# Kernel optimization log

Hardware: AMD Instinct MI355X
Metric: run time of the kernel (lower is better)

Reference implementation:

```python
import jax, jax.numpy as jnp
import numpy as np

N_EMBD = 1024
N_HEAD = 16
R = 16
SCALING = 1.0 / 16.0  # loralib default lora_alpha=1, scaling = alpha/r


def lora_linear(x, W, b, A, B):
    # loralib: y = x @ W.T + b + (x @ A.T) @ B.T * scaling
    return x @ W.T + b + (x @ A.T) @ B.T * SCALING


def setup_inputs() -> dict:
    key = jax.random.key(0)
    ks = jax.random.split(key, 16)
    B, T, S, C = 8, 1024, 256, N_EMBD
    std = 0.02
    return {
        "x": jax.random.normal(ks[0], (B, T, C), jnp.float32),
        "feature": jax.random.normal(ks[1], (B, S, C), jnp.float32),
        # c_attn (q projection)
        "Wq": jax.random.normal(ks[2], (C, C), jnp.float32) * std,
        "bq": jnp.zeros((C,), jnp.float32),
        "Aq": jax.random.normal(ks[3], (R, C), jnp.float32) * std,
        "Bq": jnp.zeros((C, R), jnp.float32),
        # feature_attn (kv projection)
        "Wf": jax.random.normal(ks[4], (2 * C, C), jnp.float32) * std,
        "bf": jnp.zeros((2 * C,), jnp.float32),
        "Af": jax.random.normal(ks[5], (R, C), jnp.float32) * std,
        "Bf": jnp.zeros((2 * C, R), jnp.float32),
        # c_proj
        "Wp": jax.random.normal(ks[6], (C, C), jnp.float32) * std,
        "bp": jnp.zeros((C,), jnp.float32),
        "Ap": jax.random.normal(ks[7], (R, C), jnp.float32) * std,
        "Bp": jnp.zeros((C, R), jnp.float32),
    }


def reference(x, feature, Wq, bq, Aq, Bq, Wf, bf, Af, Bf, Wp, bp, Ap, Bp):
    Bsz, T, C = x.shape
    S = feature.shape[1]
    H = N_HEAD
    D = C // H

    q = lora_linear(x, Wq, bq, Aq, Bq).reshape(Bsz, T, H, D).transpose(0, 2, 1, 3)
    kv = lora_linear(feature, Wf, bf, Af, Bf)
    k, v = kv[..., :C], kv[..., C:]
    k = k.reshape(Bsz, S, H, D).transpose(0, 2, 1, 3)
    v = v.reshape(Bsz, S, H, D).transpose(0, 2, 1, 3)

    att = jnp.einsum("bhtd,bhsd->bhts", q, k) * (1.0 / np.sqrt(D))
    mask = jnp.tril(jnp.ones((T, S), bool))  # bias[:, :, :T, :S]
    att = jnp.where(mask, att, -jnp.inf)
    att = jax.nn.softmax(att, axis=-1)

    y = jnp.einsum("bhts,bhsd->bhtd", att, v)
    y = y.transpose(0, 2, 1, 3).reshape(Bsz, T, C)
    return lora_linear(y, Wp, bp, Ap, Bp)
```

## Files before the change

### kernel.cpp

```cpp
#include <hip/hip_runtime.h>
#include <hip/hip_bf16.h>
#include <stdint.h>
#include <stddef.h>

typedef __hip_bfloat16 bf16;
typedef __attribute__((ext_vector_type(8))) short short8;
typedef __attribute__((ext_vector_type(4))) float floatx4;

__device__ __forceinline__ void async_load16(const bf16* g, bf16* l) {
#if defined(__has_builtin) && __has_builtin(__builtin_amdgcn_global_load_lds)
  __builtin_amdgcn_global_load_lds((__attribute__((address_space(1))) void*)g,
                                   (__attribute__((address_space(3))) void*)l,
                                   16, 0, 0);
#else
  *(short8*)l = *(const short8*)g;
#endif
}

__device__ __forceinline__ int wave_detect_f32(const unsigned short* __restrict__ xr) {
  const int lane = threadIdx.x & 63;
  const unsigned short u = xr[lane];
  const int e = (u >> 7) & 0xFF;
  const unsigned long long m = __ballot(e >= 0x93);
  return (__popcll(m) > 5) ? 1 : 0;
}

__device__ __forceinline__ float ldf(const void* p, int i, int flg) {
  return flg ? ((const float*)p)[i] : __bfloat162float(((const bf16*)p)[i]);
}

struct PrepArgs {
  const void *x, *ft, *bq, *bf, *bp;
  const void *Wq, *Aq, *Bq, *Wf, *Af, *Bf, *Wp, *Ap, *Bp;
  bf16 *cx, *cft, *cbq, *cbf, *cbp, *weffq, *wefff, *weffp;
};

__device__ __forceinline__ void canon4(const void* src, bf16* dst, int i4, int flg) {
  if (flg) {
    const float4 v = ((const float4*)src)[i4];
    dst[i4 * 4 + 0] = __float2bfloat16(v.x);
    dst[i4 * 4 + 1] = __float2bfloat16(v.y);
    dst[i4 * 4 + 2] = __float2bfloat16(v.z);
    dst[i4 * 4 + 3] = __float2bfloat16(v.w);
  } else {
    ((uint2*)dst)[i4] = ((const uint2*)src)[i4];
  }
}

__device__ __forceinline__ void weff1(const void* W, const void* Bm, const void* Am,
                                      bf16* dst, int idx, int flg) {
  const int n = idx >> 10, k = idx & 1023;
  float acc = 0.f;
#pragma unroll
  for (int r = 0; r < 16; ++r)
    acc += ldf(Bm, n * 16 + r, flg) * ldf(Am, r * 1024 + k, flg);
  dst[idx] = __float2bfloat16(ldf(W, idx, flg) + 0.0625f * acc);
}

__global__ __launch_bounds__(256) void prep_kernel(PrepArgs a) {
  const int flg = wave_detect_f32((const unsigned short*)a.x);
  const int bid = blockIdx.x, tid = threadIdx.x;
  if (bid < 8192) {
    canon4(a.x, a.cx, bid * 256 + tid, flg);
  } else if (bid < 10240) {
    canon4(a.ft, a.cft, (bid - 8192) * 256 + tid, flg);
  } else if (bid < 10241) {
    canon4(a.bq, a.cbq, tid, flg);
  } else if (bid < 10243) {
    canon4(a.bf, a.cbf, (bid - 10241) * 256 + tid, flg);
  } else if (bid < 10244) {
    canon4(a.bp, a.cbp, tid, flg);
  } else if (bid < 14340) {
    weff1(a.Wq, a.Bq, a.Aq, a.weffq, (bid - 10244) * 256 + tid, flg);
  } else if (bid < 22532) {
    weff1(a.Wf, a.Bf, a.Af, a.wefff, (bid - 14340) * 256 + tid, flg);
  } else {
    weff1(a.Wp, a.Bp, a.Ap, a.weffp, (bid - 22532) * 256 + tid, flg);
  }
}

#define GSLOT ((256 + 128) * 64)

__device__ __forceinline__ void stage_slot(const bf16* __restrict__ gA,
                                           const bf16* __restrict__ gB,
                                           bf16* slot, int tid) {
#pragma unroll
  for (int l = 0; l < 4; ++l) {
    const int D = l * 512 + tid;
    const int r = D >> 3;
    const int c = (D & 7) ^ (r & 7);
    async_load16(gA + (size_t)r * 1024 + c * 8, slot + D * 8);
  }
#pragma unroll
  for (int l = 0; l < 2; ++l) {
    const int D = l * 512 + tid;
    const int r = D >> 3;
    const int c = (D & 7) ^ (r & 7);
    async_load16(gB + (size_t)r * 1024 + c * 8, slot + 256 * 64 + D * 8);
  }
}

__device__ __forceinline__ void gemm_core(const bf16* __restrict__ A,
                                          const bf16* __restrict__ Bt,
                                          int bm, int bn, bf16* sT,
                                          floatx4 (&acc)[4][4]) {
  const int tid = threadIdx.x;
  const int wave = tid >> 6, lane = tid & 63;
  const int lrow = lane & 15, quad = lane >> 4;
  const int wm64 = (wave >> 1) << 6;
  const int wn64 = (wave & 1) << 6;
  const int pc0 = (quad ^ (lrow & 7)) << 3;

  const bf16* gA = A + (size_t)bm * 1024;
  const bf16* gB = Bt + (size_t)bn * 1024;

  stage_slot(gA, gB, sT, tid);
  stage_slot(gA + 64, gB + 64, sT + GSLOT, tid);

#pragma unroll
  for (int t = 0; t < 16; ++t) {
    asm volatile("s_waitcnt lgkmcnt(0)" ::: "memory");
    __builtin_amdgcn_s_barrier();
    __builtin_amdgcn_sched_barrier(0);
    if (t < 14) {
      stage_slot(gA + (t + 2) * 64, gB + (t + 2) * 64,
                 sT + ((t + 2) % 3) * GSLOT, tid);
      asm volatile("s_waitcnt vmcnt(12)" ::: "memory");
    } else if (t == 14) {
      asm volatile("s_waitcnt vmcnt(6)" ::: "memory");
    } else {
      asm volatile("s_waitcnt vmcnt(0)" ::: "memory");
    }
    __builtin_amdgcn_s_barrier();
    __builtin_amdgcn_sched_barrier(0);

    const bf16* slotA = sT + (t % 3) * GSLOT;
    const bf16* slotB = slotA + 256 * 64;
    short8 a_[4][2], b_[4][2];
#pragma unroll
    for (int i = 0; i < 4; ++i) {
      const bf16* ra = slotA + (wm64 + i * 16 + lrow) * 64;
      a_[i][0] = *(const short8*)(ra + pc0);
      a_[i][1] = *(const short8*)(ra + (pc0 ^ 32));
      const bf16* rb = slotB + (wn64 + i * 16 + lrow) * 64;
      b_[i][0] = *(const short8*)(rb + pc0);
      b_[i][1] = *(const short8*)(rb + (pc0 ^ 32));
    }
    __builtin_amdgcn_s_setprio(1);
#pragma unroll
    for (int kh = 0; kh < 2; ++kh)
#pragma unroll
      for (int i = 0; i < 4; ++i)
#pragma unroll
        for (int j = 0; j < 4; ++j)
          acc[i][j] = __builtin_amdgcn_mfma_f32_16x16x32_bf16(
              a_[i][kh], b_[j][kh], acc[i][j], 0, 0, 0);
    __builtin_amdgcn_s_setprio(0);
  }
}

__global__ __launch_bounds__(512, 2) void gemm_qkv(
    const bf16* __restrict__ cx, const bf16* __restrict__ cft,
    const bf16* __restrict__ weffq, const bf16* __restrict__ wefff,
    const bf16* __restrict__ cbq, const bf16* __restrict__ cbf,
    bf16* __restrict__ qws, bf16* __restrict__ kws, bf16* __restrict__ vtws) {
  __shared__ __align__(16) bf16 sT[3 * GSLOT];
  const int bid = blockIdx.x;
  int mode, bm, bn;
  const bf16 *A, *Bt, *bias;
  if (bid < 256) {
    mode = 0; A = cx; Bt = weffq; bias = cbq;
    bm = (bid >> 3) * 256; bn = (bid & 7) * 128;
  } else {
    const int b2 = bid - 256;
    mode = 1; A = cft; Bt = wefff; bias = cbf;
    bm = (b2 >> 4) * 256; bn = (b2 & 15) * 128;
  }

  const floatx4 zero4 = {0.f, 0.f, 0.f, 0.f};
  floatx4 acc[4][4];
#pragma unroll
  for (int i = 0; i < 4; ++i)
#pragma unroll
    for (int j = 0; j < 4; ++j) acc[i][j] = zero4;

  gemm_core(A, Bt, bm, bn, sT, acc);

  const int tid = threadIdx.x, wave = tid >> 6, lane = tid & 63;
  const int lrow = lane & 15, quad = lane >> 4;
  const int wm64 = (wave >> 1) << 6, wn64 = (wave & 1) << 6;
#pragma unroll
  for (int i = 0; i < 4; ++i) {
    const int mbase = bm + wm64 + i * 16 + quad * 4;
#pragma unroll
    for (int j = 0; j < 4; ++j) {
      const int n = bn + wn64 + j * 16 + lrow;
      const float bv = __bfloat162float(bias[n]);
#pragma unroll
      for (int r = 0; r < 4; ++r) {
        const int m = mbase + r;
        const bf16 hval = __float2bfloat16(acc[i][j][r] + bv);
        if (mode == 0) {
          const int b = m >> 10, t = m & 1023, hh = n >> 6, d = n & 63;
          qws[(((size_t)(b * 16 + hh)) * 1024 + t) * 64 + d] = hval;
        } else {
          const int b = m >> 8, s = m & 255;
          if (n < 1024) {
            const int hh = n >> 6, d = n & 63;
            kws[(((size_t)(b * 16 + hh)) * 256 + s) * 64 + d] = hval;
          } else {
            const int nn = n - 1024, hh = nn >> 6, d = nn & 63;
            vtws[(((size_t)(b * 16 + hh)) * 64 + d) * 256 + s] = hval;
          }
        }
      }
    }
  }
}

__global__ __launch_bounds__(512, 2) void gemm_out(
    const bf16* __restrict__ A, const bf16* __restrict__ Bt,
    const bf16* __restrict__ bias, void* __restrict__ out0,
    const unsigned short* __restrict__ xraw) {
  __shared__ __align__(16) bf16 sT[3 * GSLOT];
  const int bid = blockIdx.x;
  const int bm = (bid >> 3) * 256, bn = (bid & 7) * 128;
  const int N = 1024;

  const floatx4 zero4 = {0.f, 0.f, 0.f, 0.f};
  floatx4 acc[4][4];
#pragma unroll
  for (int i = 0; i < 4; ++i)
#pragma unroll
    for (int j = 0; j < 4; ++j) acc[i][j] = zero4;

  gemm_core(A, Bt, bm, bn, sT, acc);

  const int tid = threadIdx.x, wave = tid >> 6, lane = tid & 63;
  const int lrow = lane & 15, quad = lane >> 4;
  const int wm64 = (wave >> 1) << 6, wn64 = (wave & 1) << 6;
  const int flg = wave_detect_f32(xraw);
#pragma unroll
  for (int i = 0; i < 4; ++i) {
    const int mbase = bm + wm64 + i * 16 + quad * 4;
#pragma unroll
    for (int j = 0; j < 4; ++j) {
      const int n = bn + wn64 + j * 16 + lrow;
      const float bv = __bfloat162float(bias[n]);
#pragma unroll
      for (int r = 0; r < 4; ++r) {
        const int m = mbase + r;
        const float fval = acc[i][j][r] + bv;
        const size_t idx = (size_t)m * N + n;
        if (flg) ((float*)out0)[idx] = fval;
        else     ((bf16*)out0)[idx] = __float2bfloat16(fval);
      }
    }
  }
}

#define SKP 72
#define SVP 264
__global__ __launch_bounds__(512, 2) void attn_kernel(
    const bf16* __restrict__ qws, const bf16* __restrict__ kws,
    const bf16* __restrict__ vtws, bf16* __restrict__ yws) {
  const int b = blockIdx.z, h = blockIdx.y, qc = blockIdx.x;
  const int bh = b * 16 + h;
  __shared__ __align__(16) bf16 sK[256 * SKP];
  __shared__ __align__(16) bf16 sVt[64 * SVP];
  __shared__ __align__(16) bf16 sP[8][16 * SVP];
  const int tid = threadIdx.x, wave = tid >> 6, lane = tid & 63;
  const int lrow = lane & 15, quad = lane >> 4;
  const bf16* kg = kws + (size_t)bh * (256 * 64);
  const bf16* vg = vtws + (size_t)bh * (64 * 256);
#pragma unroll
  for (int i = 0; i < 4; ++i) {
    const int idx = i * 512 + tid;
    const int kr = idx >> 3, kc = (idx & 7) * 8;
    *(short8*)(sK + kr * SKP + kc) = *(const short8*)(kg + kr * 64 + kc);
    const int vr = idx >> 5, vc = (idx & 31) * 8;
    *(short8*)(sVt + vr * SVP + vc) = *(const short8*)(vg + vr * 256 + vc);
  }
  __syncthreads();
  bf16* sPw = sP[wave];
  const floatx4 zero4 = {0.f, 0.f, 0.f, 0.f};
  const float kscale = 0.18033688011112042f;

  for (int st = 0; st < 4; ++st) {
    const int t0 = qc * 512 + wave * 64 + st * 16;
    const bf16* qrow = qws + ((size_t)bh * 1024 + t0 + lrow) * 64;
    const short8 aq0 = *(const short8*)(qrow + quad * 8);
    const short8 aq1 = *(const short8*)(qrow + 32 + quad * 8);
    floatx4 sc[16];
#pragma unroll
    for (int nt = 0; nt < 16; ++nt) {
      floatx4 c = zero4;
      c = __builtin_amdgcn_mfma_f32_16x16x32_bf16(
          aq0, *(const short8*)(sK + (nt * 16 + lrow) * SKP + quad * 8), c, 0, 0, 0);
      c = __builtin_amdgcn_mfma_f32_16x16x32_bf16(
          aq1, *(const short8*)(sK + (nt * 16 + lrow) * SKP + 32 + quad * 8), c, 0, 0, 0);
      sc[nt] = c;
    }
    float sum[4] = {0.f, 0.f, 0.f, 0.f};
#pragma unroll
    for (int nt = 0; nt < 16; ++nt) {
      const int s = nt * 16 + lrow;
#pragma unroll
      for (int r = 0; r < 4; ++r) {
        const int t = t0 + quad * 4 + r;
        const float p = (s <= t) ? exp2f(sc[nt][r] * kscale) : 0.f;
        sum[r] += p;
        sPw[(quad * 4 + r) * SVP + nt * 16 + lrow] = __float2bfloat16(p);
      }
    }
#pragma unroll
    for (int r = 0; r < 4; ++r) {
      sum[r] += __shfl_xor(sum[r], 1, 16);
      sum[r] += __shfl_xor(sum[r], 2, 16);
      sum[r] += __shfl_xor(sum[r], 4, 16);
      sum[r] += __shfl_xor(sum[r], 8, 16);
    }
    asm volatile("s_waitcnt lgkmcnt(0)" ::: "memory");
    floatx4 ya[4];
#pragma unroll
    for (int nt = 0; nt < 4; ++nt) ya[nt] = zero4;
#pragma unroll
    for (int ks = 0; ks < 8; ++ks) {
      const short8 ap = *(const short8*)(sPw + lrow * SVP + ks * 32 + quad * 8);
#pragma unroll
      for (int nt = 0; nt < 4; ++nt)
        ya[nt] = __builtin_amdgcn_mfma_f32_16x16x32_bf16(
            ap, *(const short8*)(sVt + (nt * 16 + lrow) * SVP + ks * 32 + quad * 8),
            ya[nt], 0, 0, 0);
    }
#pragma unroll
    for (int r = 0; r < 4; ++r) {
      const float rl = 1.f / sum[r];
      const int t = t0 + quad * 4 + r;
#pragma unroll
      for (int nt = 0; nt < 4; ++nt)
        yws[((size_t)b * 1024 + t) * 1024 + h * 64 + nt * 16 + lrow] =
            __float2bfloat16(ya[nt][r] * rl);
    }
  }
}

extern "C" void kernel_launch(void* const* d_in, const int* in_sizes, int n_in,
                              void* d_out, int out_size, void* d_ws, size_t ws_size,
                              hipStream_t stream) {
  char* p = (char*)d_ws;
  bf16* cbq   = (bf16*)p;     p += 4096;
  bf16* cbf   = (bf16*)p;     p += 8192;
  bf16* cbp   = (bf16*)p;     p += 4096;
  bf16* weffq = (bf16*)p;     p += (size_t)1024 * 1024 * 2;
  bf16* wefff = (bf16*)p;     p += (size_t)2048 * 1024 * 2;
  bf16* weffp = (bf16*)p;     p += (size_t)1024 * 1024 * 2;
  bf16* qws   = (bf16*)p;     p += (size_t)8 * 16 * 1024 * 64 * 2;
  bf16* kws   = (bf16*)p;     p += (size_t)8 * 16 * 256 * 64 * 2;
  bf16* vtws  = (bf16*)p;     p += (size_t)8 * 16 * 64 * 256 * 2;
  bf16* cft   = (bf16*)p;     p += (size_t)8 * 256 * 1024 * 2;
  bf16* cx    = (bf16*)p;     p += (size_t)8 * 1024 * 1024 * 2;
  bf16* yws   = cx;
  const size_t required = (size_t)(p - (char*)d_ws);
  if (ws_size < required) return;

  PrepArgs pa;
  pa.x = d_in[0]; pa.ft = d_in[1];
  pa.bq = d_in[3]; pa.bf = d_in[7]; pa.bp = d_in[11];
  pa.Wq = d_in[2];  pa.Aq = d_in[4];  pa.Bq = d_in[5];
  pa.Wf = d_in[6];  pa.Af = d_in[8];  pa.Bf = d_in[9];
  pa.Wp = d_in[10]; pa.Ap = d_in[12]; pa.Bp = d_in[13];
  pa.cx = cx; pa.cft = cft; pa.cbq = cbq; pa.cbf = cbf; pa.cbp = cbp;
  pa.weffq = weffq; pa.wefff = wefff; pa.weffp = weffp;
  prep_kernel<<<26628, 256, 0, stream>>>(pa);

  gemm_qkv<<<384, 512, 0, stream>>>(cx, cft, weffq, wefff, cbq, cbf, qws, kws, vtws);
  attn_kernel<<<dim3(2, 16, 8), 512, 0, stream>>>(qws, kws, vtws, yws);
  gemm_out<<<256, 512, 0, stream>>>(yws, weffp, cbp, d_out, (const unsigned short*)d_in[0]);
}
```

Baseline: 241.1 us.

## Shrink GEMM tiles to 128x128 with BK32 and remap block order

Both projection GEMMs move from 256x128 tiles with a K-step of 64 and 512 threads to 128x128 tiles with a K-step of 32 and 256 threads. The LDS swizzle, the triple-buffer slot size and the vmcnt wait counts are adjusted to match. Block indices are remapped so consecutive blocks walk along M for a fixed N column, which is meant to improve weight reuse in L2. The grids double, aiming for better CU occupancy and wave balance, at the cost of twice as many barrier iterations per tile and less operand reuse per tile.

```diff
diff --git a/kernel.cpp b/kernel.cpp
--- a/kernel.cpp
+++ b/kernel.cpp
@@ -79,24 +79,24 @@
   }
 }
 
-#define GSLOT ((256 + 128) * 64)
+#define SLOT ((128 + 128) * 32)
 
 __device__ __forceinline__ void stage_slot(const bf16* __restrict__ gA,
                                            const bf16* __restrict__ gB,
                                            bf16* slot, int tid) {
 #pragma unroll
-  for (int l = 0; l < 4; ++l) {
-    const int D = l * 512 + tid;
-    const int r = D >> 3;
-    const int c = (D & 7) ^ (r & 7);
+  for (int l = 0; l < 2; ++l) {
+    const int D = l * 256 + tid;
+    const int r = D >> 2;
+    const int c = (D & 3) ^ ((r >> 1) & 3);
     async_load16(gA + (size_t)r * 1024 + c * 8, slot + D * 8);
   }
 #pragma unroll
   for (int l = 0; l < 2; ++l) {
-    const int D = l * 512 + tid;
-    const int r = D >> 3;
-    const int c = (D & 7) ^ (r & 7);
-    async_load16(gB + (size_t)r * 1024 + c * 8, slot + 256 * 64 + D * 8);
+    const int D = l * 256 + tid;
+    const int r = D >> 2;
+    const int c = (D & 3) ^ ((r >> 1) & 3);
+    async_load16(gB + (size_t)r * 1024 + c * 8, slot + 128 * 32 + D * 8);
   }
 }
 
@@ -109,72 +109,68 @@
   const int lrow = lane & 15, quad = lane >> 4;
   const int wm64 = (wave >> 1) << 6;
   const int wn64 = (wave & 1) << 6;
-  const int pc0 = (quad ^ (lrow & 7)) << 3;
+  const int pc0 = ((quad ^ ((lrow >> 1) & 3)) << 3);
 
   const bf16* gA = A + (size_t)bm * 1024;
   const bf16* gB = Bt + (size_t)bn * 1024;
 
   stage_slot(gA, gB, sT, tid);
-  stage_slot(gA + 64, gB + 64, sT + GSLOT, tid);
-
-#pragma unroll
-  for (int t = 0; t < 16; ++t) {
+  stage_slot(gA + 32, gB + 32, sT + SLOT, tid);
+
+#pragma unroll
+  for (int t = 0; t < 32; ++t) {
     asm volatile("s_waitcnt lgkmcnt(0)" ::: "memory");
     __builtin_amdgcn_s_barrier();
     __builtin_amdgcn_sched_barrier(0);
-    if (t < 14) {
-      stage_slot(gA + (t + 2) * 64, gB + (t + 2) * 64,
-                 sT + ((t + 2) % 3) * GSLOT, tid);
-      asm volatile("s_waitcnt vmcnt(12)" ::: "memory");
-    } else if (t == 14) {
-      asm volatile("s_waitcnt vmcnt(6)" ::: "memory");
+    if (t < 30) {
+      stage_slot(gA + (t + 2) * 32, gB + (t + 2) * 32,
+                 sT + ((t + 2) % 3) * SLOT, tid);
+      asm volatile("s_waitcnt vmcnt(8)" ::: "memory");
+    } else if (t == 30) {
+      asm volatile("s_waitcnt vmcnt(4)" ::: "memory");
     } else {
       asm volatile("s_waitcnt vmcnt(0)" ::: "memory");
     }
     __builtin_amdgcn_s_barrier();
     __builtin_amdgcn_sched_barrier(0);
 
-    const bf16* slotA = sT + (t % 3) * GSLOT;
-    const bf16* slotB = slotA + 256 * 64;
-    short8 a_[4][2], b_[4][2];
+    const bf16* slotA = sT + (t % 3) * SLOT;
+    const bf16* slotB = slotA + 128 * 32;
+    short8 a_[4], b_[4];
 #pragma unroll
     for (int i = 0; i < 4; ++i) {
-      const bf16* ra = slotA + (wm64 + i * 16 + lrow) * 64;
-      a_[i][0] = *(const short8*)(ra + pc0);
-      a_[i][1] = *(const short8*)(ra + (pc0 ^ 32));
-      const bf16* rb = slotB + (wn64 + i * 16 + lrow) * 64;
-      b_[i][0] = *(const short8*)(rb + pc0);
-      b_[i][1] = *(const short8*)(rb + (pc0 ^ 32));
+      a_[i] = *(const short8*)(slotA + (wm64 + i * 16 + lrow) * 32 + pc0);
+      b_[i] = *(const short8*)(slotB + (wn64 + i * 16 + lrow) * 32 + pc0);
     }
     __builtin_amdgcn_s_setprio(1);
 #pragma unroll
-    for (int kh = 0; kh < 2; ++kh)
-#pragma unroll
-      for (int i = 0; i < 4; ++i)
-#pragma unroll
-        for (int j = 0; j < 4; ++j)
-          acc[i][j] = __builtin_amdgcn_mfma_f32_16x16x32_bf16(
-              a_[i][kh], b_[j][kh], acc[i][j], 0, 0, 0);
+    for (int i = 0; i < 4; ++i)
+#pragma unroll
+      for (int j = 0; j < 4; ++j)
+        acc[i][j] = __builtin_amdgcn_mfma_f32_16x16x32_bf16(
+            a_[i], b_[j], acc[i][j], 0, 0, 0);
     __builtin_amdgcn_s_setprio(0);
   }
 }
 
-__global__ __launch_bounds__(512, 2) void gemm_qkv(
+__global__ __launch_bounds__(256, 3) void gemm_qkv(
     const bf16* __restrict__ cx, const bf16* __restrict__ cft,
     const bf16* __restrict__ weffq, const bf16* __restrict__ wefff,
     const bf16* __restrict__ cbq, const bf16* __restrict__ cbf,
     bf16* __restrict__ qws, bf16* __restrict__ kws, bf16* __restrict__ vtws) {
-  __shared__ __align__(16) bf16 sT[3 * GSLOT];
+  __shared__ __align__(16) bf16 sT[3 * SLOT];
   const int bid = blockIdx.x;
   int mode, bm, bn;
   const bf16 *A, *Bt, *bias;
-  if (bid < 256) {
+  if (bid < 512) {
     mode = 0; A = cx; Bt = weffq; bias = cbq;
-    bm = (bid >> 3) * 256; bn = (bid & 7) * 128;
+    bm = (((bid & 7) << 3) | ((bid >> 3) & 7)) * 128;
+    bn = (bid >> 6) * 128;
   } else {
-    const int b2 = bid - 256;
+    const int b2 = bid - 512;
     mode = 1; A = cft; Bt = wefff; bias = cbf;
-    bm = (b2 >> 4) * 256; bn = (b2 & 15) * 128;
+    bm = (((b2 & 7) << 1) | ((b2 >> 3) & 1)) * 128;
+    bn = (b2 >> 4) * 128;
   }
 
   const floatx4 zero4 = {0.f, 0.f, 0.f, 0.f};
@@ -218,13 +214,14 @@
   }
 }
 
-__global__ __launch_bounds__(512, 2) void gemm_out(
+__global__ __launch_bounds__(256, 3) void gemm_out(
     const bf16* __restrict__ A, const bf16* __restrict__ Bt,
     const bf16* __restrict__ bias, void* __restrict__ out0,
     const unsigned short* __restrict__ xraw) {
-  __shared__ __align__(16) bf16 sT[3 * GSLOT];
+  __shared__ __align__(16) bf16 sT[3 * SLOT];
   const int bid = blockIdx.x;
-  const int bm = (bid >> 3) * 256, bn = (bid & 7) * 128;
+  const int bm = (((bid & 7) << 3) | ((bid >> 3) & 7)) * 128;
+  const int bn = (bid >> 6) * 128;
   const int N = 1024;
 
   const floatx4 zero4 = {0.f, 0.f, 0.f, 0.f};
@@ -374,7 +371,7 @@
   pa.weffq = weffq; pa.wefff = wefff; pa.weffp = weffp;
   prep_kernel<<<26628, 256, 0, stream>>>(pa);
 
-  gemm_qkv<<<384, 512, 0, stream>>>(cx, cft, weffq, wefff, cbq, cbf, qws, kws, vtws);
+  gemm_qkv<<<768, 256, 0, stream>>>(cx, cft, weffq, wefff, cbq, cbf, qws, kws, vtws);
   attn_kernel<<<dim3(2, 16, 8), 512, 0, stream>>>(qws, kws, vtws, yws);
-  gemm_out<<<256, 512, 0, stream>>>(yws, weffp, cbp, d_out, (const unsigned short*)d_in[0]);
-}
+  gemm_out<<<512, 256, 0, stream>>>(yws, weffp, cbp, d_out, (const unsigned short*)d_in[0]);
+}
```

Result: faster. 224.7 us (-6.8%).
